# Performance work log

Measured on AMD Instinct MI355X. Metric: run time of the kernel, lower is better.

Reference implementation:

```python
import jax, jax.numpy as jnp
import numpy as np

B, IN, HID, OUT = 1024, 512, 128, 64
INP1 = IN + 1  # 513, after prepending ones column


def setup_inputs() -> dict:
    key = jax.random.key(0)
    k1, k2, k3, k4, k5, k6, k7, k8 = jax.random.split(key, 8)
    s1 = 1.0 / np.sqrt(INP1 * INP1)
    s2 = 1.0 / np.sqrt(HID)
    return {
        "img": jax.random.normal(k1, (B, IN), dtype=jnp.float32),
        "tab": jax.random.normal(k2, (B, IN), dtype=jnp.float32),
        "W1": jax.random.uniform(k3, (HID, INP1 * INP1), jnp.float32, -s1, s1),
        "b1": jax.random.uniform(k4, (HID,), jnp.float32, -s1, s1),
        "W2": jax.random.uniform(k5, (HID, HID), jnp.float32, -s2, s2),
        "b2": jax.random.uniform(k6, (HID,), jnp.float32, -s2, s2),
        "W3": jax.random.uniform(k7, (OUT, HID), jnp.float32, -s2, s2),
        "b3": jax.random.uniform(k8, (OUT,), jnp.float32, -s2, s2),
    }


def reference(img, tab, W1, b1, W2, b2, W3, b3):
    ones = jnp.ones((img.shape[0], 1), dtype=img.dtype)
    x = jnp.concatenate([ones, img], axis=1)  # [B, IN+1]
    t = jnp.concatenate([ones, tab], axis=1)  # [B, IN+1]
    # batched outer product, flattened: [B, (IN+1)*(IN+1)]
    fusion = jnp.einsum("bi,bj->bij", x, t).reshape(x.shape[0], -1)
    # dropout is identity in eval mode
    y1 = fusion @ W1.T + b1
    y2 = jnp.tanh(y1 @ W2.T + b2)
    y3 = jax.nn.relu(y2 @ W3.T + b3)
    return y3
```

## Files before the change

kernel.cpp:

```cpp
#include <hip/hip_runtime.h>
#include <hip/hip_bf16.h>

typedef __bf16 bf16x8 __attribute__((ext_vector_type(8)));
typedef float f32x4 __attribute__((ext_vector_type(4)));
typedef unsigned short u16x4 __attribute__((ext_vector_type(4)));

typedef __attribute__((address_space(1))) const unsigned int gu32;
typedef __attribute__((address_space(3))) unsigned int lu32;

#define B_SZ   1024
#define IN_SZ  512
#define HID    128
#define OUT_SZ 64
#define M_TOT  65664
#define BM     64
#define BN     512
#define BK     32
#define NKT    16

static __device__ __forceinline__ unsigned short f2bf(float f) {
    __hip_bfloat16 h = __float2bfloat16(f);
    return *reinterpret_cast<unsigned short*>(&h);
}

__global__ __launch_bounds__(256) void prep_kernel(
    const float* __restrict__ img, const float* __restrict__ tab,
    unsigned short* __restrict__ tbt, float* __restrict__ xhT,
    float* __restrict__ tc)
{
    const int blk = blockIdx.x;
    for (int j = threadIdx.x; j < 512; j += 256) {
        float v = (j == 0) ? 1.0f : tab[(size_t)blk * IN_SZ + (j - 1)];
        tbt[(size_t)blk * 512 + j] = f2bf(v);
    }
    if (threadIdx.x == 0) tc[blk] = tab[(size_t)blk * IN_SZ + 511];
    if (blk < 513) {
        for (int b = threadIdx.x; b < B_SZ; b += 256)
            xhT[(size_t)blk * B_SZ + b] =
                (blk == 0) ? 1.0f : img[(size_t)b * IN_SZ + (blk - 1)];
    }
}

__global__ __launch_bounds__(512, 4) void gemm_fused(
    const float* __restrict__ w1, const unsigned short* __restrict__ tbt,
    const float* __restrict__ xhT, const float* __restrict__ tc,
    float* __restrict__ y1acc)
{
    __shared__ unsigned short Als[BM * BK];
    __shared__ unsigned short Bls[BN * BK];

    const int bm = blockIdx.x >> 1;
    const int bn = blockIdx.x & 1;
    const int m0 = bm * BM;
    const int n0 = bn * BN;
    const int tid  = threadIdx.x;
    const int wv   = tid >> 6;
    const int lane = tid & 63;
    const int l15  = lane & 15;
    const int kg   = lane >> 4;

    const int ar  = tid >> 3;
    const int ac4 = tid & 7;
    const int achunk = (ar << 2) | ((ac4 >> 1) ^ ((ar >> 1) & 3));
    unsigned short* adst = &Als[achunk * 8 + (ac4 & 1) * 4];
    const float* asrc = w1 + (size_t)(m0 + ar) * 513 + ac4 * 4;

    const unsigned short* bsrc[4];
    unsigned short* bdst[4];
    #pragma unroll
    for (int q = 0; q < 4; ++q) {
        const int p  = q * 512 + tid;
        const int r  = p >> 2;
        const int cl = (p & 3) ^ ((r >> 1) & 3);
        bsrc[q] = tbt + (size_t)(n0 + r) * 512 + cl * 8;
        bdst[q] = &Bls[(q * 512 + wv * 64) * 8];
    }

    int aoffs[4], boffs[4];
    #pragma unroll
    for (int ms = 0; ms < 4; ++ms) {
        const int row = ms * 16 + l15;
        aoffs[ms] = ((row << 2) | (kg ^ ((row >> 1) & 3))) * 8;
    }
    #pragma unroll
    for (int ns = 0; ns < 4; ++ns) {
        const int row = wv * 64 + ns * 16 + l15;
        boffs[ns] = ((row << 2) | (kg ^ ((row >> 1) & 3))) * 8;
    }

    f32x4 acc[4][4] = {};

    for (int kt = 0; kt < NKT; ++kt) {
        const int k32 = kt * BK;
        __syncthreads();
        #pragma unroll
        for (int q = 0; q < 4; ++q)
            __builtin_amdgcn_global_load_lds(
                (gu32*)(const void*)(bsrc[q] + k32),
                (lu32*)(void*)bdst[q], 16, 0, 0);
        {
            const float f0 = asrc[k32 + 0], f1 = asrc[k32 + 1];
            const float f2 = asrc[k32 + 2], f3 = asrc[k32 + 3];
            u16x4 uv;
            uv[0] = f2bf(f0); uv[1] = f2bf(f1);
            uv[2] = f2bf(f2); uv[3] = f2bf(f3);
            *reinterpret_cast<u16x4*>(adst) = uv;
        }
        __syncthreads();

        bf16x8 af[4], bfr[4];
        #pragma unroll
        for (int ms = 0; ms < 4; ++ms)
            af[ms] = *reinterpret_cast<const bf16x8*>(&Als[aoffs[ms]]);
        #pragma unroll
        for (int ns = 0; ns < 4; ++ns)
            bfr[ns] = *reinterpret_cast<const bf16x8*>(&Bls[boffs[ns]]);
        #pragma unroll
        for (int ms = 0; ms < 4; ++ms)
            #pragma unroll
            for (int ns = 0; ns < 4; ++ns)
                acc[ms][ns] = __builtin_amdgcn_mfma_f32_16x16x32_bf16(
                    af[ms], bfr[ns], acc[ms][ns], 0, 0, 0);
    }

    const int h0 = m0 / 513;
    const int mb = (h0 + 1) * 513;
    const bool cross = (mb < m0 + BM);

    float wc[4][4];
    #pragma unroll
    for (int ms = 0; ms < 4; ++ms)
        #pragma unroll
        for (int v = 0; v < 4; ++v)
            wc[ms][v] = w1[(size_t)(m0 + ms * 16 + kg * 4 + v) * 513 + 512];

    #pragma unroll
    for (int ns = 0; ns < 4; ++ns) {
        const int ncol = n0 + wv * 64 + ns * 16 + l15;
        const float tv = tc[ncol];
        float s0 = 0.f, s1 = 0.f;
        #pragma unroll
        for (int ms = 0; ms < 4; ++ms) {
            #pragma unroll
            for (int v = 0; v < 4; ++v) {
                const int m = m0 + ms * 16 + kg * 4 + v;
                const bool lo = (m < mb);
                const int i = lo ? (m - h0 * 513) : (m - mb);
                const float xv = xhT[(size_t)i * B_SZ + ncol];
                const float val = (acc[ms][ns][v] + wc[ms][v] * tv) * xv;
                if (lo) s0 += val; else s1 += val;
            }
        }
        s0 += __shfl_xor(s0, 16); s0 += __shfl_xor(s0, 32);
        if (lane < 16) atomicAdd(&y1acc[(size_t)ncol * HID + h0], s0);
        if (cross) {
            s1 += __shfl_xor(s1, 16); s1 += __shfl_xor(s1, 32);
            if (lane < 16 && (h0 + 1) < HID)
                atomicAdd(&y1acc[(size_t)ncol * HID + h0 + 1], s1);
        }
    }
}

__global__ __launch_bounds__(128) void mlp_kernel(
    const float* __restrict__ y1acc, const float* __restrict__ b1,
    const float* __restrict__ W2, const float* __restrict__ b2,
    const float* __restrict__ W3, const float* __restrict__ b3,
    float* __restrict__ out)
{
    __shared__ float y1r[HID];
    __shared__ float y2r[HID];
    const int b = blockIdx.x;
    const int h = threadIdx.x;
    y1r[h] = y1acc[(size_t)b * HID + h] + b1[h];
    __syncthreads();
    float a = b2[h];
    const float* w2r = W2 + (size_t)h * HID;
    #pragma unroll 8
    for (int k = 0; k < HID; ++k) a += w2r[k] * y1r[k];
    y2r[h] = tanhf(a);
    __syncthreads();
    if (h < OUT_SZ) {
        float a3 = b3[h];
        const float* w3r = W3 + (size_t)h * HID;
        #pragma unroll 8
        for (int k = 0; k < HID; ++k) a3 += w3r[k] * y2r[k];
        out[(size_t)b * OUT_SZ + h] = fmaxf(a3, 0.f);
    }
}

extern "C" void kernel_launch(void* const* d_in, const int* in_sizes, int n_in,
                              void* d_out, int out_size, void* d_ws, size_t ws_size,
                              hipStream_t stream) {
    const float* img = (const float*)d_in[0];
    const float* tab = (const float*)d_in[1];
    const float* W1  = (const float*)d_in[2];
    const float* b1  = (const float*)d_in[3];
    const float* W2  = (const float*)d_in[4];
    const float* b2  = (const float*)d_in[5];
    const float* W3  = (const float*)d_in[6];
    const float* b3  = (const float*)d_in[7];
    float* out = (float*)d_out;

    char* ws = (char*)d_ws;
    float*          y1acc = (float*)ws;
    unsigned short* tbt   = (unsigned short*)(ws + 524288);
    float*          xhT   = (float*)(ws + 1572864);
    float*          tc    = (float*)(ws + 3674112);

    hipMemsetAsync(y1acc, 0, (size_t)B_SZ * HID * sizeof(float), stream);
    prep_kernel<<<dim3(1024), dim3(256), 0, stream>>>(img, tab, tbt, xhT, tc);
    gemm_fused<<<dim3(2052), dim3(512), 0, stream>>>(W1, tbt, xhT, tc, y1acc);
    mlp_kernel<<<dim3(1024), dim3(128), 0, stream>>>(y1acc, b1, W2, b2, W3, b3, out);
}
```

Baseline: 216.1 us.

## Double-buffer GEMM tiles and stream fp32 W1 straight into LDS

```diff
diff --git a/kernel.cpp b/kernel.cpp
--- a/kernel.cpp
+++ b/kernel.cpp
@@ -3,7 +3,7 @@
 
 typedef __bf16 bf16x8 __attribute__((ext_vector_type(8)));
 typedef float f32x4 __attribute__((ext_vector_type(4)));
-typedef unsigned short u16x4 __attribute__((ext_vector_type(4)));
+typedef unsigned short u16x8 __attribute__((ext_vector_type(8)));
 
 typedef __attribute__((address_space(1))) const unsigned int gu32;
 typedef __attribute__((address_space(3))) unsigned int lu32;
@@ -12,7 +12,6 @@
 #define IN_SZ  512
 #define HID    128
 #define OUT_SZ 64
-#define M_TOT  65664
 #define BM     64
 #define BN     512
 #define BK     32
@@ -46,8 +45,8 @@
     const float* __restrict__ xhT, const float* __restrict__ tc,
     float* __restrict__ y1acc)
 {
-    __shared__ unsigned short Als[BM * BK];
-    __shared__ unsigned short Bls[BN * BK];
+    __shared__ float          Afs[2][BM * BK];
+    __shared__ unsigned short Bls[2][BN * BK];
 
     const int bm = blockIdx.x >> 1;
     const int bn = blockIdx.x & 1;
@@ -60,68 +59,81 @@
     const int kg   = lane >> 4;
 
     const int ar  = tid >> 3;
-    const int ac4 = tid & 7;
-    const int achunk = (ar << 2) | ((ac4 >> 1) ^ ((ar >> 1) & 3));
-    unsigned short* adst = &Als[achunk * 8 + (ac4 & 1) * 4];
-    const float* asrc = w1 + (size_t)(m0 + ar) * 513 + ac4 * 4;
+    const int acl = (tid & 7) ^ (ar & 7);
+    const float* asrc = w1 + (size_t)(m0 + ar) * 513 + acl * 4;
+    const int aBase = (wv * 64) * 4;
 
     const unsigned short* bsrc[4];
-    unsigned short* bdst[4];
+    int bBase[4];
     #pragma unroll
     for (int q = 0; q < 4; ++q) {
         const int p  = q * 512 + tid;
         const int r  = p >> 2;
         const int cl = (p & 3) ^ ((r >> 1) & 3);
         bsrc[q] = tbt + (size_t)(n0 + r) * 512 + cl * 8;
-        bdst[q] = &Bls[(q * 512 + wv * 64) * 8];
-    }
-
-    int aoffs[4], boffs[4];
+        bBase[q] = (q * 512 + wv * 64) * 8;
+    }
+
+    int aoff0[4], aoff1[4], boffs[4];
     #pragma unroll
     for (int ms = 0; ms < 4; ++ms) {
-        const int row = ms * 16 + l15;
-        aoffs[ms] = ((row << 2) | (kg ^ ((row >> 1) & 3))) * 8;
+        const int r = ms * 16 + l15;
+        aoff0[ms] = r * 32 + (((kg * 2) + 0) ^ (r & 7)) * 4;
+        aoff1[ms] = r * 32 + (((kg * 2) + 1) ^ (r & 7)) * 4;
     }
     #pragma unroll
     for (int ns = 0; ns < 4; ++ns) {
-        const int row = wv * 64 + ns * 16 + l15;
-        boffs[ns] = ((row << 2) | (kg ^ ((row >> 1) & 3))) * 8;
+        const int r = wv * 64 + ns * 16 + l15;
+        boffs[ns] = ((r << 2) | (kg ^ ((r >> 1) & 3))) * 8;
     }
 
     f32x4 acc[4][4] = {};
 
+#define STAGE(BUF, KT) do {                                                  \
+        const int k32_ = (KT) * BK;                                          \
+        _Pragma("unroll")                                                    \
+        for (int q_ = 0; q_ < 4; ++q_)                                       \
+            __builtin_amdgcn_global_load_lds(                                \
+                (gu32*)(const void*)(bsrc[q_] + k32_),                       \
+                (lu32*)(void*)&Bls[BUF][bBase[q_]], 16, 0, 0);               \
+        __builtin_amdgcn_global_load_lds(                                    \
+            (gu32*)(const void*)(asrc + k32_),                               \
+            (lu32*)(void*)&Afs[BUF][aBase], 16, 0, 0);                       \
+    } while (0)
+
+    STAGE(0, 0);
+    __syncthreads();
+
     for (int kt = 0; kt < NKT; ++kt) {
-        const int k32 = kt * BK;
-        __syncthreads();
-        #pragma unroll
-        for (int q = 0; q < 4; ++q)
-            __builtin_amdgcn_global_load_lds(
-                (gu32*)(const void*)(bsrc[q] + k32),
-                (lu32*)(void*)bdst[q], 16, 0, 0);
-        {
-            const float f0 = asrc[k32 + 0], f1 = asrc[k32 + 1];
-            const float f2 = asrc[k32 + 2], f3 = asrc[k32 + 3];
-            u16x4 uv;
-            uv[0] = f2bf(f0); uv[1] = f2bf(f1);
-            uv[2] = f2bf(f2); uv[3] = f2bf(f3);
-            *reinterpret_cast<u16x4*>(adst) = uv;
-        }
-        __syncthreads();
-
-        bf16x8 af[4], bfr[4];
-        #pragma unroll
-        for (int ms = 0; ms < 4; ++ms)
-            af[ms] = *reinterpret_cast<const bf16x8*>(&Als[aoffs[ms]]);
+        const int cur = kt & 1;
+        if (kt + 1 < NKT) STAGE(cur ^ 1, kt + 1);
+
+        const float*          ab = &Afs[cur][0];
+        const unsigned short* bb = &Bls[cur][0];
+
+        bf16x8 bfr[4];
         #pragma unroll
         for (int ns = 0; ns < 4; ++ns)
-            bfr[ns] = *reinterpret_cast<const bf16x8*>(&Bls[boffs[ns]]);
-        #pragma unroll
-        for (int ms = 0; ms < 4; ++ms)
+            bfr[ns] = *reinterpret_cast<const bf16x8*>(&bb[boffs[ns]]);
+
+        #pragma unroll
+        for (int ms = 0; ms < 4; ++ms) {
+            const f32x4 lo = *reinterpret_cast<const f32x4*>(&ab[aoff0[ms]]);
+            const f32x4 hi = *reinterpret_cast<const f32x4*>(&ab[aoff1[ms]]);
+            u16x8 u;
+            u[0] = f2bf(lo[0]); u[1] = f2bf(lo[1]);
+            u[2] = f2bf(lo[2]); u[3] = f2bf(lo[3]);
+            u[4] = f2bf(hi[0]); u[5] = f2bf(hi[1]);
+            u[6] = f2bf(hi[2]); u[7] = f2bf(hi[3]);
+            const bf16x8 af = __builtin_bit_cast(bf16x8, u);
             #pragma unroll
             for (int ns = 0; ns < 4; ++ns)
                 acc[ms][ns] = __builtin_amdgcn_mfma_f32_16x16x32_bf16(
-                    af[ms], bfr[ns], acc[ms][ns], 0, 0, 0);
-    }
+                    af, bfr[ns], acc[ms][ns], 0, 0, 0);
+        }
+        __syncthreads();
+    }
+#undef STAGE
 
     const int h0 = m0 / 513;
     const int mb = (h0 + 1) * 513;
```

New measurement: 201.4 us. 1.07x faster.
